# Performance work log

Hardware: AMD Instinct MI355X
Metric: run time of the kernel (lower is better)

The kernel has to match this reference:

```python
import jax, jax.numpy as jnp
import numpy as np

B, C, H, W = 64, 1, 512, 512
NUM_GT = 128
PULL_W, PUSH_W = 0.25, 0.25
MARGIN = 1.0


def setup_inputs() -> dict:
    key = jax.random.key(0)
    k1, k2, k3 = jax.random.split(key, 3)
    pred = jax.random.normal(k1, (B, C, H, W), dtype=jnp.float32)
    target = jax.random.normal(k2, (B, C, H, W), dtype=jnp.float32)
    # match[b, g] = [[tl_y, tl_x], [br_y, br_x]] on the feature map
    match = jax.random.randint(k3, (B, NUM_GT, 2, 2), 0, H, dtype=jnp.int64)
    return {"pred": pred, "target": target, "match": match}


def _ae_loss_per_image(tl_preds, br_preds, m):
    # tl_preds/br_preds: [C, H, W]; m: [G, 2, 2] int coords
    ty, tx = m[:, 0, 0], m[:, 0, 1]
    by, bx = m[:, 1, 0], m[:, 1, 1]
    # gather per-box embeddings; original flattens channels into the box axis
    tl = tl_preds[:, ty, tx].T.reshape(-1)  # [G*C]
    br = br_preds[:, by, bx].T.reshape(-1)  # [G*C]
    me = (tl + br) * 0.5
    N = tl.shape[0]
    pull = jnp.sum((tl - me) ** 2 + (br - me) ** 2) / N
    # push: pairwise confusion matrix with zeroed diagonal
    d = me[:, None] - me[None, :]  # [N, N] (M=1 after flatten)
    conf = (1.0 - jnp.eye(N, dtype=me.dtype)) * (MARGIN - jnp.abs(d))
    push = jnp.sum(jax.nn.relu(conf)) / (N * (N - 1))
    return pull, push


def reference(pred, target, match):
    pulls, pushes = jax.vmap(_ae_loss_per_image)(pred, target, match)
    pull_all = PULL_W * jnp.sum(pulls)
    push_all = PUSH_W * jnp.sum(pushes)
    return pull_all, push_all
```

## Files before the change

kernel.cpp:

```cpp
#include <hip/hip_runtime.h>


#define AE_B      64
#define AE_NGT    128
#define AE_H      512
#define AE_W      512
#define AE_HW     (AE_H * AE_W)

__global__ __launch_bounds__(AE_NGT) void ae_loss_per_image(
    const float* __restrict__ pred,
    const float* __restrict__ target,
    const int*   __restrict__ match,
    float*       __restrict__ partials)
{
    const int b = blockIdx.x;
    const int t = threadIdx.x;

    __shared__ float s_me[AE_NGT];
    __shared__ float s_red[4];

    const int4 m = reinterpret_cast<const int4*>(match)[b * AE_NGT + t];
    const float tl = pred  [b * AE_HW + m.x * AE_W + m.y];
    const float br = target[b * AE_HW + m.z * AE_W + m.w];
    const float me = 0.5f * (tl + br);

    const float dtl = tl - me;
    const float dbr = br - me;
    float pull = dtl * dtl + dbr * dbr;

    s_me[t] = me;
    __syncthreads();

    float push = 0.0f;
#pragma unroll
    for (int j = 0; j < AE_NGT; ++j) {
        const float v = 1.0f - fabsf(me - s_me[j]);
        if (j != t) push += fmaxf(v, 0.0f);
    }

#pragma unroll
    for (int off = 32; off > 0; off >>= 1) {
        pull += __shfl_down(pull, off, 64);
        push += __shfl_down(push, off, 64);
    }
    const int wave = t >> 6;
    if ((t & 63) == 0) {
        s_red[wave * 2 + 0] = pull;
        s_red[wave * 2 + 1] = push;
    }
    __syncthreads();
    if (t == 0) {
        const float psum = s_red[0] + s_red[2];
        const float qsum = s_red[1] + s_red[3];
        partials[b * 2 + 0] = 0.25f * psum * (1.0f / 128.0f);
        partials[b * 2 + 1] = 0.25f * qsum * (1.0f / (128.0f * 127.0f));
    }
}

__global__ __launch_bounds__(64) void ae_loss_final(
    const float* __restrict__ partials,
    float*       __restrict__ out)
{
    const int t = threadIdx.x;
    const float2 pq = reinterpret_cast<const float2*>(partials)[t];
    float p = pq.x, q = pq.y;
#pragma unroll
    for (int off = 32; off > 0; off >>= 1) {
        p += __shfl_down(p, off, 64);
        q += __shfl_down(q, off, 64);
    }
    if (t == 0) {
        out[0] = p;
        out[1] = q;
    }
}

extern "C" void kernel_launch(void* const* d_in, const int* in_sizes, int n_in,
                              void* d_out, int out_size, void* d_ws, size_t ws_size,
                              hipStream_t stream) {
    const float* pred   = (const float*)d_in[0];
    const float* target = (const float*)d_in[1];
    const int*   match  = (const int*)d_in[2];
    float* out = (float*)d_out;
    float* partials = (float*)d_ws;

    ae_loss_per_image<<<AE_B, AE_NGT, 0, stream>>>(pred, target, match, partials);
    ae_loss_final<<<1, 64, 0, stream>>>(partials, out);
}
```

Measured before the change: 11.30 us.

## Fuse final reduction into per-image kernel via flag-based spin wait

Merges the two launches into one kernel. Blocks 1..63 publish their partial sums and set a release flag, and block 0's first wave spin-waits on those flags, reduces, and writes the final output. This removes the second kernel launch and the gap between kernels. The scheme assumes all 64 blocks are co-resident, because block 0 spins until the others finish, and it relies on the workspace flags being reset to zero after each use.

After: 10.86 us. -4.0%, faster.

```diff
diff --git a/kernel.cpp b/kernel.cpp
--- a/kernel.cpp
+++ b/kernel.cpp
@@ -3,15 +3,17 @@
 
 #define AE_B      64
 #define AE_NGT    128
-#define AE_H      512
 #define AE_W      512
-#define AE_HW     (AE_H * AE_W)
+#define AE_HW     (512 * 512)
+#define AE_MAGIC  0x5EEDF00DCAFEBABEull
 
-__global__ __launch_bounds__(AE_NGT) void ae_loss_per_image(
+__global__ __launch_bounds__(AE_NGT) void ae_loss_fused(
     const float* __restrict__ pred,
     const float* __restrict__ target,
     const int*   __restrict__ match,
-    float*       __restrict__ partials)
+    float*       __restrict__ out,
+    float*       __restrict__ partials,
+    unsigned long long* __restrict__ flags)
 {
     const int b = blockIdx.x;
     const int t = threadIdx.x;
@@ -43,35 +45,50 @@
         pull += __shfl_down(pull, off, 64);
         push += __shfl_down(push, off, 64);
     }
-    const int wave = t >> 6;
     if ((t & 63) == 0) {
-        s_red[wave * 2 + 0] = pull;
-        s_red[wave * 2 + 1] = push;
+        s_red[(t >> 6) * 2 + 0] = pull;
+        s_red[(t >> 6) * 2 + 1] = push;
     }
     __syncthreads();
+
+    if (b != 0) {
+        if (t == 0) {
+            const float2 pq = make_float2(s_red[0] + s_red[2],
+                                          s_red[1] + s_red[3]);
+            reinterpret_cast<float2*>(partials)[b] = pq;
+            __threadfence();
+            __hip_atomic_store(&flags[b], AE_MAGIC,
+                               __ATOMIC_RELEASE, __HIP_MEMORY_SCOPE_AGENT);
+        }
+        return;
+    }
+
+    if (t >= 64) return;
+
+    float p, q;
     if (t == 0) {
-        const float psum = s_red[0] + s_red[2];
-        const float qsum = s_red[1] + s_red[3];
-        partials[b * 2 + 0] = 0.25f * psum * (1.0f / 128.0f);
-        partials[b * 2 + 1] = 0.25f * qsum * (1.0f / (128.0f * 127.0f));
+        p = s_red[0] + s_red[2];
+        q = s_red[1] + s_red[3];
+    } else {
+        while (__hip_atomic_load(&flags[t], __ATOMIC_ACQUIRE,
+                                 __HIP_MEMORY_SCOPE_AGENT) != AE_MAGIC) {
+            __builtin_amdgcn_s_sleep(1);
+        }
+        const float2 pq = reinterpret_cast<const float2*>(partials)[t];
+        p = pq.x;
+        q = pq.y;
+        __hip_atomic_store(&flags[t], 0ull,
+                           __ATOMIC_RELAXED, __HIP_MEMORY_SCOPE_AGENT);
     }
-}
 
-__global__ __launch_bounds__(64) void ae_loss_final(
-    const float* __restrict__ partials,
-    float*       __restrict__ out)
-{
-    const int t = threadIdx.x;
-    const float2 pq = reinterpret_cast<const float2*>(partials)[t];
-    float p = pq.x, q = pq.y;
 #pragma unroll
     for (int off = 32; off > 0; off >>= 1) {
         p += __shfl_down(p, off, 64);
         q += __shfl_down(q, off, 64);
     }
     if (t == 0) {
-        out[0] = p;
-        out[1] = q;
+        out[0] = p * (0.25f / 128.0f);
+        out[1] = q * (0.25f / (128.0f * 127.0f));
     }
 }
 
@@ -82,8 +99,11 @@
     const float* target = (const float*)d_in[1];
     const int*   match  = (const int*)d_in[2];
     float* out = (float*)d_out;
+
     float* partials = (float*)d_ws;
+    unsigned long long* flags =
+        (unsigned long long*)((char*)d_ws + 512);
 
-    ae_loss_per_image<<<AE_B, AE_NGT, 0, stream>>>(pred, target, match, partials);
-    ae_loss_final<<<1, 64, 0, stream>>>(partials, out);
+    ae_loss_fused<<<AE_B, AE_NGT, 0, stream>>>(pred, target, match,
+                                               out, partials, flags);
 }
```
